# Optimization experiments

Hardware: AMD Instinct MI355X
Metric: run time of the kernel (lower is better)

## Reference

```python
import jax, jax.numpy as jnp
import numpy as np

HEAD_SIZE = 64


def setup_inputs() -> dict:
    key = jax.random.key(0)
    ks = jax.random.split(key, 6)
    B, S, D, H = 8, 2048, 1024, HEAD_SIZE
    return {
        "q": jax.random.normal(ks[0], (B, S, D), dtype=jnp.float32),
        "k": jax.random.normal(ks[1], (B, S, D), dtype=jnp.float32),
        "v": jax.random.normal(ks[2], (B, S, D), dtype=jnp.float32),
        "mask": jnp.ones((B, S), dtype=bool),
        "Wq": jax.random.normal(ks[3], (D, H), dtype=jnp.float32) * (D ** -0.5),
        "Wk": jax.random.normal(ks[4], (D, H), dtype=jnp.float32) * (D ** -0.5),
        "Wv": jax.random.normal(ks[5], (D, H), dtype=jnp.float32) * (D ** -0.5),
    }


def reference(q, k, v, mask, Wq, Wk, Wv):
    # Linear projections (bias=False): x @ W, W is [n_embd, head_size]
    qp = jnp.einsum("bsd,dh->bsh", q, Wq)
    kp = jnp.einsum("bsd,dh->bsh", k, Wk)
    vp = jnp.einsum("bsd,dh->bsh", v, Wv)
    scale = HEAD_SIZE ** -0.5
    scores = jnp.einsum("bqh,bkh->bqk", qp, kp) * scale  # [B, Sq, Sk]
    # 2-D mask [B, Sk] -> broadcast over query dim (mask.unsqueeze(1))
    scores = jnp.where(mask[:, None, :], scores, -jnp.inf)
    attn = jax.nn.softmax(scores, axis=-1)
    # dropout is identity in eval mode (deterministic reference)
    out = jnp.einsum("bqk,bkh->bqh", attn, vp)
    return out
```

## Files before the change

### kernel.cpp

```cpp
#include <hip/hip_runtime.h>
#include <hip/hip_bf16.h>
#include <math.h>

#define B_ 8
#define S_ 2048
#define D_ 1024
#define H_ 64
#define M_ (B_*S_)
#define SPLIT 4
#define KPS (S_/SPLIT)

typedef __attribute__((ext_vector_type(8))) short bf16x8;
typedef __attribute__((ext_vector_type(8))) unsigned short u16x8;
typedef __attribute__((ext_vector_type(4))) float f32x4;

__device__ inline unsigned short f2bf(float f) {
    unsigned int u = __builtin_bit_cast(unsigned int, f);
    u += 0x7fffu + ((u >> 16) & 1u);
    return (unsigned short)(u >> 16);
}

__device__ inline void async16(const void* g, void* l) {
    __builtin_amdgcn_global_load_lds((const __attribute__((address_space(1))) void*)g,
                                     (__attribute__((address_space(3))) void*)l, 16, 0, 0);
}

__global__ __launch_bounds__(256) void mask_kernel(const unsigned char* __restrict__ mask,
                                                   float* __restrict__ mmul, int n) {
    int j = blockIdx.x * 256 + threadIdx.x;
    if (j >= n) return;
    bool boolLayout = mask[1] != 0;
    int mv = boolLayout ? (int)mask[j] : ((const int*)mask)[j];
    mmul[j] = mv ? 1.0f : 0.0f;
}

__global__ __launch_bounds__(256) void wprep_kernel(
    const float* __restrict__ Wq, const float* __restrict__ Wk, const float* __restrict__ Wv,
    unsigned short* __restrict__ Wt)
{
    const int m = blockIdx.y;
    const float* W = (m == 0) ? Wq : (m == 1) ? Wk : Wv;
    unsigned short* Wo = Wt + (size_t)m * 64 * 1024;
    __shared__ unsigned short T[64][65];
    const int t = threadIdx.x;
    const int k0 = blockIdx.x * 64;
    #pragma unroll
    for (int i = 0; i < 16; i++) {
        int vi = t + i * 256;
        int kk = vi >> 6, n = vi & 63;
        T[kk][n] = f2bf(W[(size_t)(k0 + kk) * 64 + n]);
    }
    __syncthreads();
    #pragma unroll
    for (int i = 0; i < 4; i++) {
        int vi = t + i * 256;
        int n = vi >> 4, k4 = vi & 15;
        ushort4 u;
        u.x = T[k4*4+0][n]; u.y = T[k4*4+1][n]; u.z = T[k4*4+2][n]; u.w = T[k4*4+3][n];
        *(ushort4*)&Wo[(size_t)n * 1024 + k0 + k4*4] = u;
    }
}

__global__ __launch_bounds__(256) void proj_kernel(
    const float* __restrict__ q, const float* __restrict__ kx, const float* __restrict__ vx,
    const unsigned short* __restrict__ Wt,
    unsigned short* __restrict__ qp, unsigned short* __restrict__ kp, unsigned short* __restrict__ vpT)
{
    __shared__ unsigned short Bb[4][64 * 32];

    const int m = blockIdx.y;
    const float* x = (m == 0) ? q : (m == 1) ? kx : vx;
    const unsigned short* Wm = Wt + (size_t)m * 64 * 1024;

    const int t = threadIdx.x;
    const int w = t >> 6, l = t & 63;
    const int lrow = l & 15, quad = l >> 4;
    const int row0 = blockIdx.x * 64;

    const float* xa = x + (size_t)(row0 + w * 16 + lrow) * D_ + quad * 8;

    const int bn = t >> 2, bu = t & 3;
    const unsigned short* wsrc = Wm + (size_t)bn * 1024 + (bu ^ (bn & 3)) * 8;

    const int runit = (quad ^ (lrow & 3)) * 8;

    f32x4 acc[4] = {};
    f32x4 pa0[4], pa1[4];

#define ISSUE_B(kc, buf) do { \
    async16(wsrc + (kc) * 32, &Bb[buf][t * 8]); \
    asm volatile("" ::: "memory"); } while (0)

#define LOAD_A(st, kc) do { \
    pa0[st] = *(const f32x4*)(xa + (kc) * 32); \
    pa1[st] = *(const f32x4*)(xa + (kc) * 32 + 4); \
    asm volatile("" ::: "memory"); } while (0)

#define COMPUTE(st, buf) do { \
    f32x4 a0_ = pa0[st], a1_ = pa1[st]; \
    bf16x8 af_; \
    af_[0] = (short)f2bf(a0_.x); af_[1] = (short)f2bf(a0_.y); \
    af_[2] = (short)f2bf(a0_.z); af_[3] = (short)f2bf(a0_.w); \
    af_[4] = (short)f2bf(a1_.x); af_[5] = (short)f2bf(a1_.y); \
    af_[6] = (short)f2bf(a1_.z); af_[7] = (short)f2bf(a1_.w); \
    bf16x8 b0_ = *(const bf16x8*)&Bb[buf][0 * 512 + lrow * 32 + runit]; \
    bf16x8 b1_ = *(const bf16x8*)&Bb[buf][1 * 512 + lrow * 32 + runit]; \
    bf16x8 b2_ = *(const bf16x8*)&Bb[buf][2 * 512 + lrow * 32 + runit]; \
    bf16x8 b3_ = *(const bf16x8*)&Bb[buf][3 * 512 + lrow * 32 + runit]; \
    acc[0] = __builtin_amdgcn_mfma_f32_16x16x32_bf16(af_, b0_, acc[0], 0, 0, 0); \
    acc[1] = __builtin_amdgcn_mfma_f32_16x16x32_bf16(af_, b1_, acc[1], 0, 0, 0); \
    acc[2] = __builtin_amdgcn_mfma_f32_16x16x32_bf16(af_, b2_, acc[2], 0, 0, 0); \
    acc[3] = __builtin_amdgcn_mfma_f32_16x16x32_bf16(af_, b3_, acc[3], 0, 0, 0); } while (0)

    ISSUE_B(0, 0); LOAD_A(0, 0);
    ISSUE_B(1, 1); LOAD_A(1, 1);
    ISSUE_B(2, 2); LOAD_A(2, 2);
    LOAD_A(3, 3);

    asm volatile("s_waitcnt vmcnt(0)\n\ts_barrier" ::: "memory");
    ISSUE_B(3, 3);
    COMPUTE(0, 0);
    LOAD_A(0, 4);

    #pragma unroll 1
    for (int ob = 0; ob < 6; ++ob) {
        const int kb = ob * 4 + 1;
        #pragma unroll
        for (int kk = 0; kk < 4; ++kk) {
            const int kc = kb + kk;
            const int st = (kk + 1) & 3;
            asm volatile("s_waitcnt vmcnt(8)\n\ts_barrier" ::: "memory");
            ISSUE_B(kc + 3, (st + 3) & 3);
            COMPUTE(st, st);
            LOAD_A(st, kc + 4);
        }
    }
    asm volatile("s_waitcnt vmcnt(8)\n\ts_barrier" ::: "memory");
    ISSUE_B(28, 0); COMPUTE(1, 1); LOAD_A(1, 29);
    asm volatile("s_waitcnt vmcnt(8)\n\ts_barrier" ::: "memory");
    ISSUE_B(29, 1); COMPUTE(2, 2); LOAD_A(2, 30);
    asm volatile("s_waitcnt vmcnt(8)\n\ts_barrier" ::: "memory");
    ISSUE_B(30, 2); COMPUTE(3, 3); LOAD_A(3, 31);
    asm volatile("s_waitcnt vmcnt(8)\n\ts_barrier" ::: "memory");
    ISSUE_B(31, 3);
    COMPUTE(0, 0);
    asm volatile("s_waitcnt vmcnt(0)\n\ts_barrier" ::: "memory");
    COMPUTE(1, 1);
    COMPUTE(2, 2);
    COMPUTE(3, 3);

#undef ISSUE_B
#undef LOAD_A
#undef COMPUTE

    const int orow = row0 + w * 16 + quad * 4;
    if (m < 2) {
        unsigned short* outp = (m == 0) ? qp : kp;
        const float sc = (m == 0) ? 0.125f : 1.0f;
        #pragma unroll
        for (int c = 0; c < 4; c++)
            #pragma unroll
            for (int rr = 0; rr < 4; rr++)
                outp[(size_t)(orow + rr) * H_ + c * 16 + lrow] = f2bf(acc[c][rr] * sc);
    } else {
        const int bb = orow >> 11;
        const int s0 = orow & (S_ - 1);
        #pragma unroll
        for (int c = 0; c < 4; c++) {
            ushort4 u;
            u.x = f2bf(acc[c][0]); u.y = f2bf(acc[c][1]);
            u.z = f2bf(acc[c][2]); u.w = f2bf(acc[c][3]);
            *(ushort4*)&vpT[((size_t)bb * H_ + c * 16 + lrow) * S_ + s0] = u;
        }
    }
}

__global__ __launch_bounds__(256) void attn_kernel(
    const unsigned short* __restrict__ qp, const unsigned short* __restrict__ kp,
    const unsigned short* __restrict__ vpT, const float* __restrict__ mmul,
    float* __restrict__ po, float* __restrict__ pl)
{
    __shared__ unsigned short Qs[64][72];
    __shared__ unsigned short Ps[64][72];
    __shared__ unsigned short Ks[64 * 64];
    __shared__ unsigned short Vt[64 * 64];

    const int t = threadIdx.x;
    const int w = t >> 6, l = t & 63;
    const int lrow = l & 15, quad = l >> 4;
    const int b = blockIdx.y, q0 = blockIdx.x * 64, split = blockIdx.z;
    const int key0 = split * KPS;
    const size_t basebs = (size_t)b * S_;
    const unsigned short* vb = vpT + (size_t)b * H_ * S_;

    #pragma unroll
    for (int i = 0; i < 2; i++) {
        int p = t + i * 256;
        int r = p >> 3, c8 = p & 7;
        u16x8 u = *(const u16x8*)&qp[(basebs + q0 + r) * H_ + c8 * 8];
        *(u16x8*)&Qs[r][c8 * 8] = u;
    }

    float lsum[4] = {0.f, 0.f, 0.f, 0.f};
    f32x4 o[4] = {};

    for (int kt = 0; kt < KPS / 64; kt++) {
        const int k0 = key0 + kt * 64;
        __syncthreads();
        #pragma unroll
        for (int j = 0; j < 2; j++) {
            int p = (w * 2 + j) * 64 + l;
            int r = p >> 3;
            int c8 = (p & 7) ^ (r & 7);
            async16(&kp[(basebs + k0 + r) * H_ + c8 * 8], &Ks[p * 8]);
        }
        #pragma unroll
        for (int j = 0; j < 2; j++) {
            int p = (w * 2 + j) * 64 + l;
            int h = p >> 3;
            int c8 = (p & 7) ^ (h & 7);
            async16(&vb[(size_t)h * S_ + k0 + c8 * 8], &Vt[p * 8]);
        }
        float mm[4];
        #pragma unroll
        for (int c = 0; c < 4; c++) mm[c] = mmul[basebs + k0 + c*16 + lrow];
        __syncthreads();

        f32x4 s[4] = {};
        #pragma unroll
        for (int kk = 0; kk < 2; kk++) {
            bf16x8 aq = *(const bf16x8*)&Qs[w*16 + lrow][kk*32 + quad*8];
            #pragma unroll
            for (int c = 0; c < 4; c++) {
                const int n = c*16 + lrow;
                bf16x8 bk = *(const bf16x8*)&Ks[(n * 8 + ((kk*4 + quad) ^ (n & 7))) * 8];
                s[c] = __builtin_amdgcn_mfma_f32_16x16x32_bf16(aq, bk, s[c], 0, 0, 0);
            }
        }
        #pragma unroll
        for (int r = 0; r < 4; r++) {
            float p0 = __expf(s[0][r]) * mm[0];
            float p1 = __expf(s[1][r]) * mm[1];
            float p2 = __expf(s[2][r]) * mm[2];
            float p3 = __expf(s[3][r]) * mm[3];
            lsum[r] += (p0 + p1) + (p2 + p3);
            const int pr = w*16 + quad*4 + r;
            Ps[pr][ 0 + lrow] = f2bf(p0);
            Ps[pr][16 + lrow] = f2bf(p1);
            Ps[pr][32 + lrow] = f2bf(p2);
            Ps[pr][48 + lrow] = f2bf(p3);
        }
        #pragma unroll
        for (int kk = 0; kk < 2; kk++) {
            bf16x8 ap = *(const bf16x8*)&Ps[w*16 + lrow][kk*32 + quad*8];
            #pragma unroll
            for (int c = 0; c < 4; c++) {
                const int h = c*16 + lrow;
                bf16x8 bv = *(const bf16x8*)&Vt[(h * 8 + ((kk*4 + quad) ^ (h & 7))) * 8];
                o[c] = __builtin_amdgcn_mfma_f32_16x16x32_bf16(ap, bv, o[c], 0, 0, 0);
            }
        }
    }

    float* pob = po + (size_t)split * M_ * H_;
    float* plb = pl + (size_t)split * M_;
    #pragma unroll
    for (int r = 0; r < 4; r++) {
        #pragma unroll
        for (int d = 1; d < 16; d <<= 1)
            lsum[r] += __shfl_xor(lsum[r], d, 64);
        const size_t row = basebs + q0 + w*16 + quad*4 + r;
        if (lrow == 0) plb[row] = lsum[r];
        #pragma unroll
        for (int c = 0; c < 4; c++)
            pob[row * H_ + c*16 + lrow] = o[c][r];
    }
}

__global__ __launch_bounds__(256) void combine_kernel(
    const float* __restrict__ po, const float* __restrict__ pl, float* __restrict__ out)
{
    const int idx = blockIdx.x * 256 + threadIdx.x;
    const size_t row = idx >> 4;
    const int c4 = (idx & 15) * 4;
    float lt = 0.f;
    #pragma unroll
    for (int s = 0; s < SPLIT; s++) lt += pl[(size_t)s * M_ + row];
    f32x4 acc = {};
    #pragma unroll
    for (int s = 0; s < SPLIT; s++) {
        const f32x4 p = *(const f32x4*)&po[((size_t)s * M_ + row) * H_ + c4];
        acc += p;
    }
    const float inv = 1.0f / lt;
    f32x4 r = acc * inv;
    *(f32x4*)&out[row * H_ + c4] = r;
}

extern "C" void kernel_launch(void* const* d_in, const int* in_sizes, int n_in,
                              void* d_out, int out_size, void* d_ws, size_t ws_size,
                              hipStream_t stream) {
    const float* q  = (const float*)d_in[0];
    const float* k  = (const float*)d_in[1];
    const float* v  = (const float*)d_in[2];
    const unsigned char* mask = (const unsigned char*)d_in[3];
    const float* Wq = (const float*)d_in[4];
    const float* Wk = (const float*)d_in[5];
    const float* Wv = (const float*)d_in[6];
    float* out = (float*)d_out;

    unsigned short* qp  = (unsigned short*)d_ws;
    unsigned short* kp  = qp + (size_t)M_ * H_;
    unsigned short* vpT = kp + (size_t)M_ * H_;
    float* mmul = (float*)(vpT + (size_t)M_ * H_);
    unsigned short* Wt = (unsigned short*)(mmul + M_);
    float* po = (float*)(Wt + (size_t)3 * 64 * 1024);
    float* pl = po + (size_t)SPLIT * M_ * H_;

    wprep_kernel<<<dim3(16, 3), dim3(256), 0, stream>>>(Wq, Wk, Wv, Wt);
    mask_kernel<<<dim3((M_ + 255)/256), dim3(256), 0, stream>>>(mask, mmul, M_);
    proj_kernel<<<dim3(M_/64, 3), dim3(256), 0, stream>>>(q, k, v, Wt, qp, kp, vpT);
    attn_kernel<<<dim3(S_/64, B_, SPLIT), dim3(256), 0, stream>>>(qp, kp, vpT, mmul, po, pl);
    combine_kernel<<<dim3(M_*16/256), dim3(256), 0, stream>>>(po, pl, out);
}
```

Baseline: 243.2 us.

## Split projection GEMM along K and add a reduction kernel

The projection kernel now splits the 1024-wide reduction dimension into two halves across a third grid dimension, writing fp32 partial results to workspace. A new combine kernel sums the partials, converts to bf16, and writes Q/K and the transposed V through an LDS staging tile. The intent is to double the block count for the projection so more CUs stay busy and latency hides better. The cost is an extra launch and fp32 partial traffic through memory. The reduction loop's wait counts are also tightened at the tail.

```diff
diff --git a/kernel.cpp b/kernel.cpp
--- a/kernel.cpp
+++ b/kernel.cpp
@@ -9,6 +9,8 @@
 #define M_ (B_*S_)
 #define SPLIT 4
 #define KPS (S_/SPLIT)
+#define SPLITK 2
+#define KSEG (D_/SPLITK)
 
 typedef __attribute__((ext_vector_type(8))) short bf16x8;
 typedef __attribute__((ext_vector_type(8))) unsigned short u16x8;
@@ -64,24 +66,24 @@
 __global__ __launch_bounds__(256) void proj_kernel(
     const float* __restrict__ q, const float* __restrict__ kx, const float* __restrict__ vx,
     const unsigned short* __restrict__ Wt,
-    unsigned short* __restrict__ qp, unsigned short* __restrict__ kp, unsigned short* __restrict__ vpT)
+    float* __restrict__ pp)
 {
     __shared__ unsigned short Bb[4][64 * 32];
 
     const int m = blockIdx.y;
+    const int ks = blockIdx.z;
     const float* x = (m == 0) ? q : (m == 1) ? kx : vx;
     const unsigned short* Wm = Wt + (size_t)m * 64 * 1024;
+    const int kbase = ks * KSEG;
 
     const int t = threadIdx.x;
     const int w = t >> 6, l = t & 63;
     const int lrow = l & 15, quad = l >> 4;
     const int row0 = blockIdx.x * 64;
 
-    const float* xa = x + (size_t)(row0 + w * 16 + lrow) * D_ + quad * 8;
-
+    const float* xa = x + (size_t)(row0 + w * 16 + lrow) * D_ + kbase + quad * 8;
     const int bn = t >> 2, bu = t & 3;
-    const unsigned short* wsrc = Wm + (size_t)bn * 1024 + (bu ^ (bn & 3)) * 8;
-
+    const unsigned short* wsrc = Wm + (size_t)bn * 1024 + kbase + (bu ^ (bn & 3)) * 8;
     const int runit = (quad ^ (lrow & 3)) * 8;
 
     f32x4 acc[4] = {};
@@ -112,65 +114,99 @@
     acc[2] = __builtin_amdgcn_mfma_f32_16x16x32_bf16(af_, b2_, acc[2], 0, 0, 0); \
     acc[3] = __builtin_amdgcn_mfma_f32_16x16x32_bf16(af_, b3_, acc[3], 0, 0, 0); } while (0)
 
+#define W8 asm volatile("s_waitcnt vmcnt(8)\n\ts_barrier" ::: "memory")
+#define W6 asm volatile("s_waitcnt vmcnt(6)\n\ts_barrier" ::: "memory")
+#define W3 asm volatile("s_waitcnt vmcnt(3)\n\ts_barrier" ::: "memory")
+#define W0 asm volatile("s_waitcnt vmcnt(0)\n\ts_barrier" ::: "memory")
+
     ISSUE_B(0, 0); LOAD_A(0, 0);
     ISSUE_B(1, 1); LOAD_A(1, 1);
     ISSUE_B(2, 2); LOAD_A(2, 2);
     LOAD_A(3, 3);
 
-    asm volatile("s_waitcnt vmcnt(0)\n\ts_barrier" ::: "memory");
-    ISSUE_B(3, 3);
-    COMPUTE(0, 0);
-    LOAD_A(0, 4);
-
+    W8; ISSUE_B(3, 3);  COMPUTE(0, 0); LOAD_A(0, 4);
     #pragma unroll 1
-    for (int ob = 0; ob < 6; ++ob) {
-        const int kb = ob * 4 + 1;
+    for (int ob = 0; ob < 2; ++ob) {
         #pragma unroll
         for (int kk = 0; kk < 4; ++kk) {
-            const int kc = kb + kk;
+            const int kc = ob * 4 + kk + 1;
             const int st = (kk + 1) & 3;
-            asm volatile("s_waitcnt vmcnt(8)\n\ts_barrier" ::: "memory");
-            ISSUE_B(kc + 3, (st + 3) & 3);
-            COMPUTE(st, st);
-            LOAD_A(st, kc + 4);
-        }
-    }
-    asm volatile("s_waitcnt vmcnt(8)\n\ts_barrier" ::: "memory");
-    ISSUE_B(28, 0); COMPUTE(1, 1); LOAD_A(1, 29);
-    asm volatile("s_waitcnt vmcnt(8)\n\ts_barrier" ::: "memory");
-    ISSUE_B(29, 1); COMPUTE(2, 2); LOAD_A(2, 30);
-    asm volatile("s_waitcnt vmcnt(8)\n\ts_barrier" ::: "memory");
-    ISSUE_B(30, 2); COMPUTE(3, 3); LOAD_A(3, 31);
-    asm volatile("s_waitcnt vmcnt(8)\n\ts_barrier" ::: "memory");
-    ISSUE_B(31, 3);
-    COMPUTE(0, 0);
-    asm volatile("s_waitcnt vmcnt(0)\n\ts_barrier" ::: "memory");
-    COMPUTE(1, 1);
-    COMPUTE(2, 2);
-    COMPUTE(3, 3);
+            W8; ISSUE_B(kc + 3, (st + 3) & 3); COMPUTE(st, st); LOAD_A(st, kc + 4);
+        }
+    }
+    W8; ISSUE_B(12, 0); COMPUTE(1, 1); LOAD_A(1, 13);
+    W8; ISSUE_B(13, 1); COMPUTE(2, 2); LOAD_A(2, 14);
+    W8; ISSUE_B(14, 2); COMPUTE(3, 3); LOAD_A(3, 15);
+    W8; ISSUE_B(15, 3); COMPUTE(0, 0);
+    W6; COMPUTE(1, 1);
+    W3; COMPUTE(2, 2);
+    W0; COMPUTE(3, 3);
 
 #undef ISSUE_B
 #undef LOAD_A
 #undef COMPUTE
-
-    const int orow = row0 + w * 16 + quad * 4;
+#undef W8
+#undef W6
+#undef W3
+#undef W0
+
+    const float sc = (m == 0) ? 0.125f : 1.0f;
+    float* ppb = pp + ((size_t)(m * SPLITK + ks) * M_ + row0) * 64;
+    const int orow = w * 16 + quad * 4;
+    #pragma unroll
+    for (int c = 0; c < 4; c++)
+        #pragma unroll
+        for (int rr = 0; rr < 4; rr++)
+            ppb[(size_t)(orow + rr) * 64 + c * 16 + lrow] = acc[c][rr] * sc;
+}
+
+__global__ __launch_bounds__(256) void cproj_kernel(
+    const float* __restrict__ pp,
+    unsigned short* __restrict__ qp, unsigned short* __restrict__ kp,
+    unsigned short* __restrict__ vpT)
+{
+    __shared__ unsigned short T[64][65];
+    const int m = blockIdx.y;
+    const int r0 = blockIdx.x * 64;
+    const int t = threadIdx.x;
+    const float* p0 = pp + ((size_t)(m * SPLITK + 0) * M_ + r0) * 64;
+    const float* p1 = pp + ((size_t)(m * SPLITK + 1) * M_ + r0) * 64;
+
     if (m < 2) {
         unsigned short* outp = (m == 0) ? qp : kp;
-        const float sc = (m == 0) ? 0.125f : 1.0f;
-        #pragma unroll
-        for (int c = 0; c < 4; c++)
-            #pragma unroll
-            for (int rr = 0; rr < 4; rr++)
-                outp[(size_t)(orow + rr) * H_ + c * 16 + lrow] = f2bf(acc[c][rr] * sc);
+        #pragma unroll
+        for (int i = 0; i < 4; i++) {
+            int p = i * 256 + t;
+            int row = p >> 4, qd = p & 15;
+            f32x4 a = *(const f32x4*)&p0[(size_t)row * 64 + qd * 4];
+            f32x4 b = *(const f32x4*)&p1[(size_t)row * 64 + qd * 4];
+            f32x4 s = a + b;
+            ushort4 u;
+            u.x = f2bf(s.x); u.y = f2bf(s.y); u.z = f2bf(s.z); u.w = f2bf(s.w);
+            *(ushort4*)&outp[(size_t)(r0 + row) * H_ + qd * 4] = u;
+        }
     } else {
-        const int bb = orow >> 11;
-        const int s0 = orow & (S_ - 1);
-        #pragma unroll
-        for (int c = 0; c < 4; c++) {
+        #pragma unroll
+        for (int i = 0; i < 4; i++) {
+            int p = i * 256 + t;
+            int row = p >> 4, qd = p & 15;
+            f32x4 a = *(const f32x4*)&p0[(size_t)row * 64 + qd * 4];
+            f32x4 b = *(const f32x4*)&p1[(size_t)row * 64 + qd * 4];
+            f32x4 s = a + b;
+            T[row][qd*4+0] = f2bf(s.x); T[row][qd*4+1] = f2bf(s.y);
+            T[row][qd*4+2] = f2bf(s.z); T[row][qd*4+3] = f2bf(s.w);
+        }
+        __syncthreads();
+        const int bb = r0 >> 11;
+        const int s0 = r0 & (S_ - 1);
+        #pragma unroll
+        for (int i = 0; i < 4; i++) {
+            int p = i * 256 + t;
+            int h = p >> 4, sq = p & 15;
             ushort4 u;
-            u.x = f2bf(acc[c][0]); u.y = f2bf(acc[c][1]);
-            u.z = f2bf(acc[c][2]); u.w = f2bf(acc[c][3]);
-            *(ushort4*)&vpT[((size_t)bb * H_ + c * 16 + lrow) * S_ + s0] = u;
+            u.x = T[sq*4+0][h]; u.y = T[sq*4+1][h];
+            u.z = T[sq*4+2][h]; u.w = T[sq*4+3][h];
+            *(ushort4*)&vpT[((size_t)bb * H_ + h) * S_ + s0 + sq*4] = u;
         }
     }
 }
@@ -314,12 +350,14 @@
     unsigned short* vpT = kp + (size_t)M_ * H_;
     float* mmul = (float*)(vpT + (size_t)M_ * H_);
     unsigned short* Wt = (unsigned short*)(mmul + M_);
-    float* po = (float*)(Wt + (size_t)3 * 64 * 1024);
+    float* pp = (float*)(Wt + (size_t)3 * 64 * 1024);
+    float* po = pp;
     float* pl = po + (size_t)SPLIT * M_ * H_;
 
     wprep_kernel<<<dim3(16, 3), dim3(256), 0, stream>>>(Wq, Wk, Wv, Wt);
     mask_kernel<<<dim3((M_ + 255)/256), dim3(256), 0, stream>>>(mask, mmul, M_);
-    proj_kernel<<<dim3(M_/64, 3), dim3(256), 0, stream>>>(q, k, v, Wt, qp, kp, vpT);
+    proj_kernel<<<dim3(M_/64, 3, SPLITK), dim3(256), 0, stream>>>(q, k, v, Wt, pp);
+    cproj_kernel<<<dim3(M_/64, 3), dim3(256), 0, stream>>>(pp, qp, kp, vpT);
     attn_kernel<<<dim3(S_/64, B_, SPLIT), dim3(256), 0, stream>>>(qp, kp, vpT, mmul, po, pl);
     combine_kernel<<<dim3(M_*16/256), dim3(256), 0, stream>>>(po, pl, out);
 }
```

After: 257.8 us. 1.06x slower.
